# Kernel tuning notes

Measured on AMD Instinct MI355X. Metric: run time of the kernel, lower is better.

The kernel has to match this reference:

```python
import jax, jax.numpy as jnp
import numpy as np

B, S, E, H = 4, 2048, 1024, 16
DH = E // H


def setup_inputs() -> dict:
    key = jax.random.key(0)
    ks = jax.random.split(key, 8)
    sc = 0.02
    inp = {
        "v": jax.random.normal(ks[0], (B, S, E), jnp.float32),
        "k": jax.random.normal(ks[1], (B, S, E), jnp.float32),
        "q": jax.random.normal(ks[2], (B, S, E), jnp.float32),
        # causal mask, broadcast over batch and heads; 0 => masked
        "mask": jnp.tril(jnp.ones((S, S), jnp.int32))[None, None, :, :],
        "wq": jax.random.normal(ks[3], (E, E), jnp.float32) * sc,
        "bq": jnp.zeros((E,), jnp.float32),
        "wk": jax.random.normal(ks[4], (E, E), jnp.float32) * sc,
        "bk": jnp.zeros((E,), jnp.float32),
        "wv": jax.random.normal(ks[5], (E, E), jnp.float32) * sc,
        "bv": jnp.zeros((E,), jnp.float32),
        "wo": jax.random.normal(ks[6], (E, E), jnp.float32) * sc,
        "bo": jnp.zeros((E,), jnp.float32),
    }
    return inp


def _split_heads(x):
    # [B,S,E] -> [B,H,S,DH]
    b, s, _ = x.shape
    return x.reshape(b, s, H, DH).transpose(0, 2, 1, 3)


def reference(v, k, q, mask, wq, bq, wk, bk, wv, bv, wo, bo):
    # Linear layers (torch Linear: x @ W^T + b)
    qh = _split_heads(q @ wq.T + bq)
    kh = _split_heads(k @ wk.T + bk)
    vh = _split_heads(v @ wv.T + bv)
    scale = 1.0 / jnp.sqrt(jnp.asarray(DH, qh.dtype))
    scores = jnp.einsum("bhqd,bhkd->bhqk", qh, kh) * scale  # [B,H,S,S]
    scores = jnp.where(mask == 0, -jnp.inf, scores)
    attn = jax.nn.softmax(scores, axis=-1)
    # dropout p=0.0 -> identity
    x = jnp.einsum("bhqk,bhkd->bhqd", attn, vh)  # [B,H,S,DH]
    x = x.transpose(0, 2, 1, 3).reshape(x.shape[0], -1, E)  # [B,S,E]
    return x @ wo.T + bo
```

## Files before the change

kernel.cpp:

```cpp
#include <hip/hip_runtime.h>
#include <hip/hip_bf16.h>

#define B_  4
#define S_  2048
#define E_  1024
#define H_  16
#define DH_ 64
constexpr int M_ = B_ * S_;
constexpr int K_ = E_;
constexpr int N_ = E_;
constexpr long NE_ = (long)B_ * S_ * E_;
constexpr long EE_ = (long)E_ * E_;

typedef __attribute__((ext_vector_type(8))) short bf16x8;
typedef __attribute__((ext_vector_type(4))) float f32x4;
typedef __attribute__((ext_vector_type(16))) float f32x16;

__device__ __forceinline__ unsigned short f2bf(float f) {
    union { float f; unsigned u; } a; a.f = f;
    unsigned u = a.u;
    return (unsigned short)((u + 0x7fffu + ((u >> 16) & 1u)) >> 16);
}
__device__ __forceinline__ unsigned short f2bf_fast(float f) {
    union { float f; unsigned u; } a; a.f = f;
    return (unsigned short)((a.u + 0x8000u) >> 16);
}

__device__ __forceinline__ void async_copy16(const unsigned short* g, unsigned short* l) {
    __builtin_amdgcn_global_load_lds(
        (const __attribute__((address_space(1))) void*)g,
        (__attribute__((address_space(3))) void*)l, 16, 0, 0);
}

__global__ void cast3(const float* __restrict__ i0, const float* __restrict__ i1,
                      const float* __restrict__ i2,
                      unsigned short* __restrict__ o0, unsigned short* __restrict__ o1,
                      unsigned short* __restrict__ o2, int n4) {
    const float* in = blockIdx.y == 0 ? i0 : (blockIdx.y == 1 ? i1 : i2);
    unsigned short* out = blockIdx.y == 0 ? o0 : (blockIdx.y == 1 ? o1 : o2);
    int i = blockIdx.x * blockDim.x + threadIdx.x;
    if (i >= n4) return;
    float4 v = ((const float4*)in)[i];
    ushort4 o;
    o.x = f2bf(v.x); o.y = f2bf(v.y); o.z = f2bf(v.z); o.w = f2bf(v.w);
    ((ushort4*)out)[i] = o;
}

__global__ void cast4(const float* __restrict__ i0, const float* __restrict__ i1,
                      const float* __restrict__ i2, const float* __restrict__ i3,
                      unsigned short* __restrict__ o0, unsigned short* __restrict__ o1,
                      unsigned short* __restrict__ o2, unsigned short* __restrict__ o3,
                      int n4) {
    int y = blockIdx.y;
    const float* in = y == 0 ? i0 : (y == 1 ? i1 : (y == 2 ? i2 : i3));
    unsigned short* out = y == 0 ? o0 : (y == 1 ? o1 : (y == 2 ? o2 : o3));
    int i = blockIdx.x * blockDim.x + threadIdx.x;
    if (i >= n4) return;
    float4 v = ((const float4*)in)[i];
    ushort4 o;
    o.x = f2bf(v.x); o.y = f2bf(v.y); o.z = f2bf(v.z); o.w = f2bf(v.w);
    ((ushort4*)out)[i] = o;
}

__device__ __forceinline__ void gemm_core(
    const unsigned short* __restrict__ A, const unsigned short* __restrict__ Bw,
    unsigned short* sA, unsigned short* sB, int bm, int bn,
    int wave, int lane, f32x4 (*acc)[4]) {
    const int lane15 = lane & 15;
    const int laneq  = lane >> 4;
    const int waveM = wave & 1, waveN = wave >> 1;
    const int lrow = lane >> 3;
    const int lcol = (lane & 7) * 8;

    for (int k0 = 0; k0 < K_; k0 += 64) {
        __syncthreads();
        for (int c = wave; c < 16; c += 4) {
            const unsigned short* gA = A + (long)(bm * 128 + c * 8 + lrow) * K_ + k0 + lcol;
            async_copy16(gA, &sA[c * 512]);
            const unsigned short* gB = Bw + (long)(bn * 128 + c * 8 + lrow) * K_ + k0 + lcol;
            async_copy16(gB, &sB[c * 512]);
        }
        __syncthreads();
#pragma unroll
        for (int ks = 0; ks < 2; ++ks) {
            const int kc = ks * 32 + laneq * 8;
            bf16x8 af[4], bfr[4];
#pragma unroll
            for (int mi = 0; mi < 4; ++mi)
                af[mi] = *(const bf16x8*)&sA[(waveM * 64 + mi * 16 + lane15) * 64 + kc];
#pragma unroll
            for (int ni = 0; ni < 4; ++ni)
                bfr[ni] = *(const bf16x8*)&sB[(waveN * 64 + ni * 16 + lane15) * 64 + kc];
#pragma unroll
            for (int mi = 0; mi < 4; ++mi)
#pragma unroll
                for (int ni = 0; ni < 4; ++ni)
                    acc[mi][ni] = __builtin_amdgcn_mfma_f32_16x16x32_bf16(
                        af[mi], bfr[ni], acc[mi][ni], 0, 0, 0);
        }
    }
}

__global__ __launch_bounds__(256, 2)
void gemm3(const unsigned short* __restrict__ A0, const unsigned short* __restrict__ A1,
           const unsigned short* __restrict__ A2,
           const unsigned short* __restrict__ W0, const unsigned short* __restrict__ W1,
           const unsigned short* __restrict__ W2,
           const float* __restrict__ b0, const float* __restrict__ b1,
           const float* __restrict__ b2,
           unsigned short* __restrict__ o0, unsigned short* __restrict__ o1,
           unsigned short* __restrict__ o2, float osc0) {
    __shared__ __align__(16) unsigned short sA[128 * 64];
    __shared__ __align__(16) unsigned short sB[128 * 64];
    const int z = blockIdx.z;
    const unsigned short* A  = z == 0 ? A0 : (z == 1 ? A1 : A2);
    const unsigned short* Bw = z == 0 ? W0 : (z == 1 ? W1 : W2);
    const float* bias        = z == 0 ? b0 : (z == 1 ? b1 : b2);
    unsigned short* Out      = z == 0 ? o0 : (z == 1 ? o1 : o2);
    const float oscale = z == 0 ? osc0 : 1.0f;

    const int tid = threadIdx.x, wave = tid >> 6, lane = tid & 63;
    const int lane15 = lane & 15, laneq = lane >> 4;
    const int bm = blockIdx.x, bn = blockIdx.y;
    const int waveM = wave & 1, waveN = wave >> 1;

    f32x4 acc[4][4] = {};
    gemm_core(A, Bw, sA, sB, bm, bn, wave, lane, acc);

#pragma unroll
    for (int mi = 0; mi < 4; ++mi) {
        const int mbase = bm * 128 + waveM * 64 + mi * 16 + laneq * 4;
#pragma unroll
        for (int ni = 0; ni < 4; ++ni) {
            const int n = bn * 128 + waveN * 64 + ni * 16 + lane15;
            const float bv = bias[n];
#pragma unroll
            for (int r = 0; r < 4; ++r) {
                const int m = mbase + r;
                const float v = (acc[mi][ni][r] + bv) * oscale;
                const int b = m >> 11, s = m & (S_ - 1);
                const int h = n >> 6, d = n & (DH_ - 1);
                long idx;
                if (z == 2) idx = ((long)(b * H_ + h) * DH_ + d) * S_ + s;
                else        idx = ((long)(b * H_ + h) * S_ + s) * DH_ + d;
                Out[idx] = f2bf(v);
            }
        }
    }
}

__global__ __launch_bounds__(256, 2)
void gemm_out(const unsigned short* __restrict__ A, const unsigned short* __restrict__ Bw,
              const float* __restrict__ bias, float* __restrict__ Out) {
    __shared__ __align__(16) unsigned short sA[128 * 64];
    __shared__ __align__(16) unsigned short sB[128 * 64];
    const int tid = threadIdx.x, wave = tid >> 6, lane = tid & 63;
    const int lane15 = lane & 15, laneq = lane >> 4;
    const int bm = blockIdx.x, bn = blockIdx.y;
    const int waveM = wave & 1, waveN = wave >> 1;

    f32x4 acc[4][4] = {};
    gemm_core(A, Bw, sA, sB, bm, bn, wave, lane, acc);

#pragma unroll
    for (int mi = 0; mi < 4; ++mi) {
        const int mbase = bm * 128 + waveM * 64 + mi * 16 + laneq * 4;
#pragma unroll
        for (int ni = 0; ni < 4; ++ni) {
            const int n = bn * 128 + waveN * 64 + ni * 16 + lane15;
            const float bv = bias[n];
#pragma unroll
            for (int r = 0; r < 4; ++r)
                Out[(long)(mbase + r) * N_ + n] = acc[mi][ni][r] + bv;
        }
    }
}

constexpr int ALDK = 72;

__global__ __launch_bounds__(256, 4)
void attn_kernel(const unsigned short* __restrict__ qh,
                 const unsigned short* __restrict__ kh,
                 const unsigned short* __restrict__ vT,
                 unsigned short* __restrict__ ctx) {
    __shared__ __align__(16) unsigned short sK[64 * ALDK];
    __shared__ __align__(16) unsigned short sV[64 * ALDK];
    __shared__ __align__(16) unsigned short sP[128 * ALDK];

    const int tid = threadIdx.x;
    const int wave = tid >> 6, lane = tid & 63;
    const int l31 = lane & 31, lhi = lane >> 5;
    const int x = blockIdx.x;
    const int bh = blockIdx.y;
    const int qta = x, qtb = 31 - x;
    const bool isB = wave >= 2;
    const int qrow0 = (isB ? qtb : qta) * 64 + (wave & 1) * 32;
    const long headQ = (long)bh * S_ * DH_;
    const long headV = (long)bh * DH_ * S_;

    bf16x8 qf[4];
    {
        const unsigned short* qrow = qh + headQ + (long)(qrow0 + l31) * DH_ + lhi * 8;
        qf[0] = *(const bf16x8*)(qrow);
        qf[1] = *(const bf16x8*)(qrow + 16);
        qf[2] = *(const bf16x8*)(qrow + 32);
        qf[3] = *(const bf16x8*)(qrow + 48);
    }

    f32x16 oacc[2] = {};
    float rs[16];
#pragma unroll
    for (int i = 0; i < 16; ++i) rs[i] = 0.f;

    unsigned short* myP = sP + wave * 32 * ALDK;

    for (int kt = 0; kt <= qtb; ++kt) {
        const int k0 = kt * 64;
        __syncthreads();
        for (int it = tid; it < 512; it += 256) {
            const int row = it >> 3, col = (it & 7) * 8;
            *(bf16x8*)&sK[row * ALDK + col] =
                *(const bf16x8*)(kh + headQ + (long)(k0 + row) * DH_ + col);
            *(bf16x8*)&sV[row * ALDK + col] =
                *(const bf16x8*)(vT + headV + (long)row * S_ + k0 + col);
        }
        __syncthreads();

        if (!isB && kt > qta) continue;

        f32x16 st[2] = {};
#pragma unroll
        for (int kg = 0; kg < 2; ++kg)
#pragma unroll
            for (int ch = 0; ch < 4; ++ch) {
                bf16x8 kf = *(const bf16x8*)&sK[(kg * 32 + l31) * ALDK + ch * 16 + lhi * 8];
                st[kg] = __builtin_amdgcn_mfma_f32_32x32x16_bf16(qf[ch], kf, st[kg], 0, 0, 0);
            }

        const bool needmask = (k0 + 63 > qrow0);
#pragma unroll
        for (int kg = 0; kg < 2; ++kg) {
            const int colg = k0 + kg * 32 + l31;
#pragma unroll
            for (int i = 0; i < 16; ++i) {
                const int rloc = (i & 3) + 8 * (i >> 2) + 4 * lhi;
                float s = st[kg][i];
                if (needmask && colg > qrow0 + rloc) s = -1e30f;
                const float p = __builtin_amdgcn_exp2f(s);
                rs[i] += p;
                myP[rloc * ALDK + kg * 32 + l31] = f2bf_fast(p);
            }
        }

#pragma unroll
        for (int kc = 0; kc < 4; ++kc) {
            bf16x8 pf = *(const bf16x8*)&myP[l31 * ALDK + kc * 16 + lhi * 8];
#pragma unroll
            for (int dg = 0; dg < 2; ++dg) {
                bf16x8 vf = *(const bf16x8*)&sV[(dg * 32 + l31) * ALDK + kc * 16 + lhi * 8];
                oacc[dg] = __builtin_amdgcn_mfma_f32_32x32x16_bf16(pf, vf, oacc[dg], 0, 0, 0);
            }
        }
    }

    float rinv[16];
#pragma unroll
    for (int i = 0; i < 16; ++i) {
        float v = rs[i];
        v += __shfl_xor(v, 1); v += __shfl_xor(v, 2); v += __shfl_xor(v, 4);
        v += __shfl_xor(v, 8); v += __shfl_xor(v, 16);
        rinv[i] = 1.0f / v;
    }

    const int b = bh >> 4, h = bh & 15;
#pragma unroll
    for (int i = 0; i < 16; ++i) {
        const int rloc = (i & 3) + 8 * (i >> 2) + 4 * lhi;
        unsigned short* crow = ctx + ((long)b * S_ + qrow0 + rloc) * E_ + h * 64 + l31;
        crow[0]  = f2bf(oacc[0][i] * rinv[i]);
        crow[32] = f2bf(oacc[1][i] * rinv[i]);
    }
}

extern "C" void kernel_launch(void* const* d_in, const int* in_sizes, int n_in,
                              void* d_out, int out_size, void* d_ws, size_t ws_size,
                              hipStream_t stream) {
    const float* v_in = (const float*)d_in[0];
    const float* k_in = (const float*)d_in[1];
    const float* q_in = (const float*)d_in[2];
    const float* wq = (const float*)d_in[4];
    const float* bq = (const float*)d_in[5];
    const float* wk = (const float*)d_in[6];
    const float* bk = (const float*)d_in[7];
    const float* wv = (const float*)d_in[8];
    const float* bv = (const float*)d_in[9];
    const float* wo = (const float*)d_in[10];
    const float* bo = (const float*)d_in[11];

    unsigned short* qb   = (unsigned short*)d_ws;
    unsigned short* kb   = qb + NE_;
    unsigned short* vb   = kb + NE_;
    unsigned short* wqb  = vb + NE_;
    unsigned short* wkb  = wqb + EE_;
    unsigned short* wvb  = wkb + EE_;
    unsigned short* wob  = wvb + EE_;
    unsigned short* qhb  = wob + EE_;
    unsigned short* khb  = qhb + NE_;
    unsigned short* vTb  = khb + NE_;
    unsigned short* ctxb = qb;

    const int n4a = (int)(NE_ / 4);
    const int n4w = (int)(EE_ / 4);
    cast3<<<dim3(n4a / 256, 3), 256, 0, stream>>>(q_in, k_in, v_in, qb, kb, vb, n4a);
    cast4<<<dim3(n4w / 256, 4), 256, 0, stream>>>(wq, wk, wv, wo, wqb, wkb, wvb, wob, n4w);

    const float QSCALE = 0.125f * 1.44269504089f;

    gemm3<<<dim3(M_ / 128, N_ / 128, 3), 256, 0, stream>>>(
        qb, kb, vb, wqb, wkb, wvb, bq, bk, bv, qhb, khb, vTb, QSCALE);

    attn_kernel<<<dim3(16, B_ * H_), 256, 0, stream>>>(qhb, khb, vTb, ctxb);

    gemm_out<<<dim3(M_ / 128, N_ / 128), 256, 0, stream>>>(ctxb, wob, bo, (float*)d_out);
}
```

Measured before the change: 398.2 us.

## Restructure causal attention: balanced per-wave work, 16x16 MFMA, double-buffered K/V prefetch

The attention kernel now has every wave process both paired query tiles (a and 31-a) with 16-row slices. Before, waves 0-1 handled tile a and sat idle once past its diagonal while waves 2-3 kept working. It switches from 32x32x16 to 16x16x32 bf16 MFMA and adds a templated diagonal/non-diagonal tile path so masking is only evaluated on the diagonal tile. K/V tiles are double-buffered, with the next tile loaded into registers during compute and written to LDS afterwards, removing one barrier per iteration. The P scratch uses an XOR swizzle to reduce bank conflicts, at the cost of more register pressure from two sets of accumulators.

New measurement: 364.3 us. 1.09x faster.

```diff
diff --git a/kernel.cpp b/kernel.cpp
--- a/kernel.cpp
+++ b/kernel.cpp
@@ -14,7 +14,6 @@
 
 typedef __attribute__((ext_vector_type(8))) short bf16x8;
 typedef __attribute__((ext_vector_type(4))) float f32x4;
-typedef __attribute__((ext_vector_type(16))) float f32x16;
 
 __device__ __forceinline__ unsigned short f2bf(float f) {
     union { float f; unsigned u; } a; a.f = f;
@@ -178,107 +177,154 @@
 
 constexpr int ALDK = 72;
 
+template <bool DIAG>
+__device__ __forceinline__ void attn_tile(
+    const bf16x8* qf, const unsigned short* sK, const unsigned short* sV,
+    unsigned short* sP, int wave, int lane15, int laneq,
+    f32x4* o_acc, float* rs) {
+    f32x4 sc[4] = {};
+#pragma unroll
+    for (int ks = 0; ks < 2; ++ks) {
+#pragma unroll
+        for (int ct = 0; ct < 4; ++ct) {
+            bf16x8 kf = *(const bf16x8*)&sK[(ct * 16 + lane15) * ALDK + ks * 32 + laneq * 8];
+            sc[ct] = __builtin_amdgcn_mfma_f32_16x16x32_bf16(qf[ks], kf, sc[ct], 0, 0, 0);
+        }
+    }
+    const int prow = wave * 16 + laneq * 4;
+#pragma unroll
+    for (int ct = 0; ct < 4; ++ct) {
+        const int colsw = ((ct ^ laneq) & 3) * 16 + lane15;
+#pragma unroll
+        for (int r = 0; r < 4; ++r) {
+            float s = sc[ct][r];
+            if (DIAG) {
+                const int colg = ct * 16 + lane15;
+                if (colg > prow + r) s = -1e30f;
+            }
+            const float p = __builtin_amdgcn_exp2f(s);
+            rs[r] += p;
+            sP[(prow + r) * ALDK + colsw] = f2bf_fast(p);
+        }
+    }
+    const int pkey = ((lane15 >> 2) & 3) * 16;
+#pragma unroll
+    for (int ks = 0; ks < 2; ++ks) {
+        const int pcol = (ks * 32 + laneq * 8) ^ pkey;
+        bf16x8 pf = *(const bf16x8*)&sP[(wave * 16 + lane15) * ALDK + pcol];
+#pragma unroll
+        for (int dt = 0; dt < 4; ++dt) {
+            bf16x8 vf = *(const bf16x8*)&sV[(dt * 16 + lane15) * ALDK + ks * 32 + laneq * 8];
+            o_acc[dt] = __builtin_amdgcn_mfma_f32_16x16x32_bf16(pf, vf, o_acc[dt], 0, 0, 0);
+        }
+    }
+}
+
 __global__ __launch_bounds__(256, 4)
 void attn_kernel(const unsigned short* __restrict__ qh,
                  const unsigned short* __restrict__ kh,
                  const unsigned short* __restrict__ vT,
                  unsigned short* __restrict__ ctx) {
-    __shared__ __align__(16) unsigned short sK[64 * ALDK];
-    __shared__ __align__(16) unsigned short sV[64 * ALDK];
-    __shared__ __align__(16) unsigned short sP[128 * ALDK];
+    __shared__ __align__(16) unsigned short sK[2][64 * ALDK];
+    __shared__ __align__(16) unsigned short sV[2][64 * ALDK];
+    __shared__ __align__(16) unsigned short sP[64 * ALDK];
 
     const int tid = threadIdx.x;
     const int wave = tid >> 6, lane = tid & 63;
-    const int l31 = lane & 31, lhi = lane >> 5;
+    const int lane15 = lane & 15, laneq = lane >> 4;
     const int x = blockIdx.x;
+    const int qta = x, qtb = 31 - x;
     const int bh = blockIdx.y;
-    const int qta = x, qtb = 31 - x;
-    const bool isB = wave >= 2;
-    const int qrow0 = (isB ? qtb : qta) * 64 + (wave & 1) * 32;
     const long headQ = (long)bh * S_ * DH_;
     const long headV = (long)bh * DH_ * S_;
-
-    bf16x8 qf[4];
+    const int q0a = qta * 64, q0b = qtb * 64;
+
+    bf16x8 qfA[2], qfB[2];
     {
-        const unsigned short* qrow = qh + headQ + (long)(qrow0 + l31) * DH_ + lhi * 8;
-        qf[0] = *(const bf16x8*)(qrow);
-        qf[1] = *(const bf16x8*)(qrow + 16);
-        qf[2] = *(const bf16x8*)(qrow + 32);
-        qf[3] = *(const bf16x8*)(qrow + 48);
-    }
-
-    f32x16 oacc[2] = {};
-    float rs[16];
-#pragma unroll
-    for (int i = 0; i < 16; ++i) rs[i] = 0.f;
-
-    unsigned short* myP = sP + wave * 32 * ALDK;
-
-    for (int kt = 0; kt <= qtb; ++kt) {
-        const int k0 = kt * 64;
+        const unsigned short* qa = qh + headQ + (long)(q0a + wave * 16 + lane15) * DH_;
+        qfA[0] = *(const bf16x8*)(qa + laneq * 8);
+        qfA[1] = *(const bf16x8*)(qa + 32 + laneq * 8);
+        const unsigned short* qbp = qh + headQ + (long)(q0b + wave * 16 + lane15) * DH_;
+        qfB[0] = *(const bf16x8*)(qbp + laneq * 8);
+        qfB[1] = *(const bf16x8*)(qbp + 32 + laneq * 8);
+    }
+
+    f32x4 oA[4] = {}, oB[4] = {};
+    float rsA[4] = {0.f, 0.f, 0.f, 0.f}, rsB[4] = {0.f, 0.f, 0.f, 0.f};
+
+    const int r0 = tid >> 3;
+    const int c0 = (tid & 7) * 8;
+
+    const int ktmax = qtb + 1;
+
+    {
+        const unsigned short* kbase = kh + headQ;
+        *(bf16x8*)&sK[0][r0 * ALDK + c0] = *(const bf16x8*)(kbase + (long)r0 * DH_ + c0);
+        *(bf16x8*)&sK[0][(32 + r0) * ALDK + c0] = *(const bf16x8*)(kbase + (long)(32 + r0) * DH_ + c0);
+        const unsigned short* vbase = vT + headV;
+        *(bf16x8*)&sV[0][r0 * ALDK + c0] = *(const bf16x8*)(vbase + (long)r0 * S_ + c0);
+        *(bf16x8*)&sV[0][(32 + r0) * ALDK + c0] = *(const bf16x8*)(vbase + (long)(32 + r0) * S_ + c0);
+    }
+
+    for (int kt = 0; kt < ktmax; ++kt) {
+        const int cur = kt & 1, nxt = cur ^ 1;
         __syncthreads();
-        for (int it = tid; it < 512; it += 256) {
-            const int row = it >> 3, col = (it & 7) * 8;
-            *(bf16x8*)&sK[row * ALDK + col] =
-                *(const bf16x8*)(kh + headQ + (long)(k0 + row) * DH_ + col);
-            *(bf16x8*)&sV[row * ALDK + col] =
-                *(const bf16x8*)(vT + headV + (long)row * S_ + k0 + col);
-        }
-        __syncthreads();
-
-        if (!isB && kt > qta) continue;
-
-        f32x16 st[2] = {};
-#pragma unroll
-        for (int kg = 0; kg < 2; ++kg)
-#pragma unroll
-            for (int ch = 0; ch < 4; ++ch) {
-                bf16x8 kf = *(const bf16x8*)&sK[(kg * 32 + l31) * ALDK + ch * 16 + lhi * 8];
-                st[kg] = __builtin_amdgcn_mfma_f32_32x32x16_bf16(qf[ch], kf, st[kg], 0, 0, 0);
-            }
-
-        const bool needmask = (k0 + 63 > qrow0);
-#pragma unroll
-        for (int kg = 0; kg < 2; ++kg) {
-            const int colg = k0 + kg * 32 + l31;
-#pragma unroll
-            for (int i = 0; i < 16; ++i) {
-                const int rloc = (i & 3) + 8 * (i >> 2) + 4 * lhi;
-                float s = st[kg][i];
-                if (needmask && colg > qrow0 + rloc) s = -1e30f;
-                const float p = __builtin_amdgcn_exp2f(s);
-                rs[i] += p;
-                myP[rloc * ALDK + kg * 32 + l31] = f2bf_fast(p);
-            }
-        }
-
-#pragma unroll
-        for (int kc = 0; kc < 4; ++kc) {
-            bf16x8 pf = *(const bf16x8*)&myP[l31 * ALDK + kc * 16 + lhi * 8];
-#pragma unroll
-            for (int dg = 0; dg < 2; ++dg) {
-                bf16x8 vf = *(const bf16x8*)&sV[(dg * 32 + l31) * ALDK + kc * 16 + lhi * 8];
-                oacc[dg] = __builtin_amdgcn_mfma_f32_32x32x16_bf16(pf, vf, oacc[dg], 0, 0, 0);
-            }
-        }
-    }
-
-    float rinv[16];
-#pragma unroll
-    for (int i = 0; i < 16; ++i) {
-        float v = rs[i];
-        v += __shfl_xor(v, 1); v += __shfl_xor(v, 2); v += __shfl_xor(v, 4);
-        v += __shfl_xor(v, 8); v += __shfl_xor(v, 16);
-        rinv[i] = 1.0f / v;
+
+        bf16x8 kr0, kr1, vr0, vr1;
+        const bool pfn = (kt + 1 < ktmax);
+        if (pfn) {
+            const int k0n = (kt + 1) * 64;
+            const unsigned short* kbase = kh + headQ + (long)k0n * DH_;
+            kr0 = *(const bf16x8*)(kbase + (long)r0 * DH_ + c0);
+            kr1 = *(const bf16x8*)(kbase + (long)(32 + r0) * DH_ + c0);
+            const unsigned short* vbase = vT + headV + k0n;
+            vr0 = *(const bf16x8*)(vbase + (long)r0 * S_ + c0);
+            vr1 = *(const bf16x8*)(vbase + (long)(32 + r0) * S_ + c0);
+        }
+
+        if (kt == qtb)
+            attn_tile<true >(qfB, sK[cur], sV[cur], sP, wave, lane15, laneq, oB, rsB);
+        else
+            attn_tile<false>(qfB, sK[cur], sV[cur], sP, wave, lane15, laneq, oB, rsB);
+
+        if (kt <= qta) {
+            if (kt == qta)
+                attn_tile<true >(qfA, sK[cur], sV[cur], sP, wave, lane15, laneq, oA, rsA);
+            else
+                attn_tile<false>(qfA, sK[cur], sV[cur], sP, wave, lane15, laneq, oA, rsA);
+        }
+
+        if (pfn) {
+            *(bf16x8*)&sK[nxt][r0 * ALDK + c0] = kr0;
+            *(bf16x8*)&sK[nxt][(32 + r0) * ALDK + c0] = kr1;
+            *(bf16x8*)&sV[nxt][r0 * ALDK + c0] = vr0;
+            *(bf16x8*)&sV[nxt][(32 + r0) * ALDK + c0] = vr1;
+        }
+    }
+
+    float lA[4], lB[4];
+#pragma unroll
+    for (int r = 0; r < 4; ++r) {
+        float va = rsA[r];
+        va += __shfl_xor(va, 1); va += __shfl_xor(va, 2);
+        va += __shfl_xor(va, 4); va += __shfl_xor(va, 8);
+        lA[r] = va;
+        float vb = rsB[r];
+        vb += __shfl_xor(vb, 1); vb += __shfl_xor(vb, 2);
+        vb += __shfl_xor(vb, 4); vb += __shfl_xor(vb, 8);
+        lB[r] = vb;
     }
 
     const int b = bh >> 4, h = bh & 15;
 #pragma unroll
-    for (int i = 0; i < 16; ++i) {
-        const int rloc = (i & 3) + 8 * (i >> 2) + 4 * lhi;
-        unsigned short* crow = ctx + ((long)b * S_ + qrow0 + rloc) * E_ + h * 64 + l31;
-        crow[0]  = f2bf(oacc[0][i] * rinv[i]);
-        crow[32] = f2bf(oacc[1][i] * rinv[i]);
+    for (int dt = 0; dt < 4; ++dt) {
+        const int d = h * 64 + dt * 16 + lane15;
+#pragma unroll
+        for (int r = 0; r < 4; ++r) {
+            const int rowo = wave * 16 + laneq * 4 + r;
+            ctx[((long)b * S_ + q0a + rowo) * E_ + d] = f2bf(oA[dt][r] / lA[r]);
+            ctx[((long)b * S_ + q0b + rowo) * E_ + d] = f2bf(oB[dt][r] / lB[r]);
+        }
     }
 }
 
```
